# Kernel tuning notes

Hardware: AMD Instinct MI355X
Metric: run time of the kernel (lower is better)

Reference implementation:

```python
import jax, jax.numpy as jnp
import numpy as np

B, T, I = 8, 8192, 128
E, J, K = 16, 128, 1024


def setup_inputs() -> dict:
    key = jax.random.key(0)
    k1, k2, k3 = jax.random.split(key, 3)
    X = jax.random.normal(k1, (B, T, I), dtype=jnp.float32)
    ind = jax.random.randint(k2, (B, E, K), 0, T, dtype=jnp.int64)
    # matches torch.rand(E, I, J): uniform [0, 1)
    W = jax.random.uniform(k3, (E, I, J), dtype=jnp.float32)
    return {"X": X, "ind": ind, "W": W}


def reference(X, ind, W):
    # Dense per-expert matmul over ALL tokens: Y[b,e,t,j] = sum_i X[b,t,i] W[e,i,j]
    # (torch expand is a broadcast view; einsum broadcasts directly)
    Y = jnp.einsum('bti,eij->betj', X, W)  # [B, E, T, J]
    # Gather selected tokens per (batch, expert) along the token axis
    Yg = jnp.take_along_axis(Y, ind[..., None], axis=2)  # [B, E, K, J]
    return Yg
```

## Files before the change

kernel.cpp:

```cpp
#include <hip/hip_runtime.h>

#define B_ 8
#define T_ 8192
#define I_ 128
#define E_ 16
#define J_ 128
#define K_ 1024
#define ROWS 128

typedef unsigned short u16;
typedef unsigned int   u32;
typedef __attribute__((ext_vector_type(8))) short s8v;
typedef __attribute__((ext_vector_type(4))) float f4v;

__device__ __forceinline__ u16 f2bf(float f) {
    union { float f; u32 u; } v; v.f = f;
    const u32 u = v.u;
    return (u16)((u + 0x7fffu + ((u >> 16) & 1u)) >> 16);
}

__global__ __launch_bounds__(512, 4)
void gather_mfma(const float* __restrict__ X, const int* __restrict__ ind,
                 const float* __restrict__ W, float* __restrict__ Y) {
    __shared__ u16 WsT[I_ * J_];
    __shared__ u16 Xs[ROWS * I_];

    const int t    = threadIdx.x;
    const int wave = t >> 6;
    const int lane = t & 63;

    const int orig = blockIdx.x;
    const int bid  = (orig & 7) * 128 + (orig >> 3);
    const int kt = bid & 7;
    const int be = bid >> 3;
    const int e  = be & (E_ - 1);
    const int b  = be >> 4;
    const int k0 = kt * ROWS;

    const int r   = t >> 2;
    const int q   = t & 3;
    const int idx = ind[(size_t)be * K_ + k0 + r];

    {
        const float* We = W + (size_t)e * (I_ * J_);
        const int io = t & 15;
        const int j0 = (t >> 4) * 4;
        float4 w4[8];
#pragma unroll
        for (int u = 0; u < 8; ++u)
            w4[u] = *reinterpret_cast<const float4*>(We + (size_t)(io * 8 + u) * J_ + j0);
#pragma unroll
        for (int qq = 0; qq < 4; ++qq) {
            const int j = j0 + qq;
            s8v o;
#pragma unroll
            for (int u = 0; u < 8; ++u) {
                const float* wf = reinterpret_cast<const float*>(&w4[u]);
                o[u] = (short)f2bf(wf[qq]);
            }
            *reinterpret_cast<s8v*>((char*)WsT + ((j * 256 + io * 16) ^ ((j & 7) << 4))) = o;
        }
    }

    {
        const float4* Xr = reinterpret_cast<const float4*>(X + ((size_t)b * T_ + idx) * I_) + q * 8;
        const int sx = (r & 7) << 4;
        char* xrow = (char*)Xs + r * 256;
#pragma unroll
        for (int u = 0; u < 4; ++u) {
            const float4 a = Xr[2 * u], c = Xr[2 * u + 1];
            s8v o;
            o[0] = (short)f2bf(a.x); o[1] = (short)f2bf(a.y);
            o[2] = (short)f2bf(a.z); o[3] = (short)f2bf(a.w);
            o[4] = (short)f2bf(c.x); o[5] = (short)f2bf(c.y);
            o[6] = (short)f2bf(c.z); o[7] = (short)f2bf(c.w);
            *reinterpret_cast<s8v*>(xrow + ((q * 64 + u * 16) ^ sx)) = o;
        }
    }
    __syncthreads();

    const int rq  = wave >> 1;
    const int jh  = wave & 1;
    const int g   = lane >> 4;
    const int l15 = lane & 15;
    const int sx  = (lane & 7) << 4;

    const char* xb = (const char*)Xs  + (size_t)(rq * 32 + l15) * 256;
    const char* wb = (const char*)WsT + (size_t)(jh * 64 + l15) * 256;

    s8v af[2][4];
#pragma unroll
    for (int s = 0; s < 4; ++s) {
        const int off = (s * 64 + g * 16) ^ sx;
        af[0][s] = *reinterpret_cast<const s8v*>(xb + off);
        af[1][s] = *reinterpret_cast<const s8v*>(xb + 16 * 256 + off);
    }

    float* Yb = Y + ((size_t)be * K_ + k0) * J_;
#pragma unroll
    for (int n = 0; n < 4; ++n) {
        f4v acc0, acc1;
#pragma unroll
        for (int rr = 0; rr < 4; ++rr) { acc0[rr] = 0.f; acc1[rr] = 0.f; }
#pragma unroll
        for (int s = 0; s < 4; ++s) {
            const int off = (s * 64 + g * 16) ^ sx;
            const s8v bf = *reinterpret_cast<const s8v*>(wb + n * 16 * 256 + off);
            acc0 = __builtin_amdgcn_mfma_f32_16x16x32_bf16(af[0][s], bf, acc0, 0, 0, 0);
            acc1 = __builtin_amdgcn_mfma_f32_16x16x32_bf16(af[1][s], bf, acc1, 0, 0, 0);
        }
        const int col = jh * 64 + n * 16 + l15;
        const int row0 = rq * 32 + g * 4;
#pragma unroll
        for (int rr = 0; rr < 4; ++rr)
            Yb[(size_t)(row0 + rr) * J_ + col] = acc0[rr];
#pragma unroll
        for (int rr = 0; rr < 4; ++rr)
            Yb[(size_t)(row0 + 16 + rr) * J_ + col] = acc1[rr];
    }
}

extern "C" void kernel_launch(void* const* d_in, const int* in_sizes, int n_in,
                              void* d_out, int out_size, void* d_ws, size_t ws_size,
                              hipStream_t stream) {
    (void)in_sizes; (void)n_in; (void)out_size; (void)d_ws; (void)ws_size;
    const float* X   = (const float*)d_in[0];
    const int*   ind = (const int*)d_in[1];
    const float* W   = (const float*)d_in[2];
    float*       Y   = (float*)d_out;

    const int grid = B_ * E_ * (K_ / ROWS);
    hipLaunchKernelGGL(gather_mfma, dim3(grid), dim3(512), 0, stream,
                       X, ind, W, Y);
}
```

Before: 28.44 us.

## Process two row tiles per block and prefetch second X gather during compute

Each block now handles 256 token rows instead of 128, which halves the grid and amortizes the W load and bf16 transpose over twice the work. The second tile's X rows are loaded into registers before the first tile's MFMA compute and store, so the gather latency overlaps the compute. The cost is fewer blocks (512 instead of 1024), which reduces parallelism and latency hiding across CUs, plus extra registers for the prefetch buffer and two more barriers.

```diff
diff --git a/kernel.cpp b/kernel.cpp
--- a/kernel.cpp
+++ b/kernel.cpp
@@ -30,16 +30,17 @@
     const int lane = t & 63;
 
     const int orig = blockIdx.x;
-    const int bid  = (orig & 7) * 128 + (orig >> 3);
-    const int kt = bid & 7;
-    const int be = bid >> 3;
+    const int bid  = (orig & 7) * 64 + (orig >> 3);
+    const int kh = bid & 3;
+    const int be = bid >> 2;
     const int e  = be & (E_ - 1);
     const int b  = be >> 4;
-    const int k0 = kt * ROWS;
+    const int k0 = kh * (2 * ROWS);
 
     const int r   = t >> 2;
     const int q   = t & 3;
-    const int idx = ind[(size_t)be * K_ + k0 + r];
+    const int idx0 = ind[(size_t)be * K_ + k0 + r];
+    const int idx1 = ind[(size_t)be * K_ + k0 + ROWS + r];
 
     {
         const float* We = W + (size_t)e * (I_ * J_);
@@ -62,21 +63,29 @@
         }
     }
 
-    {
-        const float4* Xr = reinterpret_cast<const float4*>(X + ((size_t)b * T_ + idx) * I_) + q * 8;
-        const int sx = (r & 7) << 4;
-        char* xrow = (char*)Xs + r * 256;
+    const int sxr = (r & 7) << 4;
+    char* xrow = (char*)Xs + r * 256;
+    float4 v[8];
+    auto load_rows = [&](int idxv) {
+        const float4* Xr = reinterpret_cast<const float4*>(X + ((size_t)b * T_ + idxv) * I_) + q * 8;
+#pragma unroll
+        for (int u = 0; u < 8; ++u) v[u] = Xr[u];
+    };
+    auto pack_write = [&]() {
 #pragma unroll
         for (int u = 0; u < 4; ++u) {
-            const float4 a = Xr[2 * u], c = Xr[2 * u + 1];
+            const float4 a = v[2 * u], c = v[2 * u + 1];
             s8v o;
             o[0] = (short)f2bf(a.x); o[1] = (short)f2bf(a.y);
             o[2] = (short)f2bf(a.z); o[3] = (short)f2bf(a.w);
             o[4] = (short)f2bf(c.x); o[5] = (short)f2bf(c.y);
             o[6] = (short)f2bf(c.z); o[7] = (short)f2bf(c.w);
-            *reinterpret_cast<s8v*>(xrow + ((q * 64 + u * 16) ^ sx)) = o;
+            *reinterpret_cast<s8v*>(xrow + ((q * 64 + u * 16) ^ sxr)) = o;
         }
-    }
+    };
+
+    load_rows(idx0);
+    pack_write();
     __syncthreads();
 
     const int rq  = wave >> 1;
@@ -84,40 +93,47 @@
     const int g   = lane >> 4;
     const int l15 = lane & 15;
     const int sx  = (lane & 7) << 4;
-
     const char* xb = (const char*)Xs  + (size_t)(rq * 32 + l15) * 256;
     const char* wb = (const char*)WsT + (size_t)(jh * 64 + l15) * 256;
 
-    s8v af[2][4];
-#pragma unroll
-    for (int s = 0; s < 4; ++s) {
-        const int off = (s * 64 + g * 16) ^ sx;
-        af[0][s] = *reinterpret_cast<const s8v*>(xb + off);
-        af[1][s] = *reinterpret_cast<const s8v*>(xb + 16 * 256 + off);
-    }
-
-    float* Yb = Y + ((size_t)be * K_ + k0) * J_;
-#pragma unroll
-    for (int n = 0; n < 4; ++n) {
-        f4v acc0, acc1;
-#pragma unroll
-        for (int rr = 0; rr < 4; ++rr) { acc0[rr] = 0.f; acc1[rr] = 0.f; }
+    auto compute_store = [&](int kbase) {
+        s8v af[2][4];
 #pragma unroll
         for (int s = 0; s < 4; ++s) {
             const int off = (s * 64 + g * 16) ^ sx;
-            const s8v bf = *reinterpret_cast<const s8v*>(wb + n * 16 * 256 + off);
-            acc0 = __builtin_amdgcn_mfma_f32_16x16x32_bf16(af[0][s], bf, acc0, 0, 0, 0);
-            acc1 = __builtin_amdgcn_mfma_f32_16x16x32_bf16(af[1][s], bf, acc1, 0, 0, 0);
+            af[0][s] = *reinterpret_cast<const s8v*>(xb + off);
+            af[1][s] = *reinterpret_cast<const s8v*>(xb + 16 * 256 + off);
         }
-        const int col = jh * 64 + n * 16 + l15;
-        const int row0 = rq * 32 + g * 4;
+        float* Yb = Y + ((size_t)be * K_ + kbase) * J_;
 #pragma unroll
-        for (int rr = 0; rr < 4; ++rr)
-            Yb[(size_t)(row0 + rr) * J_ + col] = acc0[rr];
+        for (int n = 0; n < 4; ++n) {
+            f4v acc0, acc1;
 #pragma unroll
-        for (int rr = 0; rr < 4; ++rr)
-            Yb[(size_t)(row0 + 16 + rr) * J_ + col] = acc1[rr];
-    }
+            for (int rr = 0; rr < 4; ++rr) { acc0[rr] = 0.f; acc1[rr] = 0.f; }
+#pragma unroll
+            for (int s = 0; s < 4; ++s) {
+                const int off = (s * 64 + g * 16) ^ sx;
+                const s8v bf = *reinterpret_cast<const s8v*>(wb + n * 16 * 256 + off);
+                acc0 = __builtin_amdgcn_mfma_f32_16x16x32_bf16(af[0][s], bf, acc0, 0, 0, 0);
+                acc1 = __builtin_amdgcn_mfma_f32_16x16x32_bf16(af[1][s], bf, acc1, 0, 0, 0);
+            }
+            const int col = jh * 64 + n * 16 + l15;
+            const int row0 = rq * 32 + g * 4;
+#pragma unroll
+            for (int rr = 0; rr < 4; ++rr)
+                Yb[(size_t)(row0 + rr) * J_ + col] = acc0[rr];
+#pragma unroll
+            for (int rr = 0; rr < 4; ++rr)
+                Yb[(size_t)(row0 + 16 + rr) * J_ + col] = acc1[rr];
+        }
+    };
+
+    load_rows(idx1);
+    compute_store(k0);
+    __syncthreads();
+    pack_write();
+    __syncthreads();
+    compute_store(k0 + ROWS);
 }
 
 extern "C" void kernel_launch(void* const* d_in, const int* in_sizes, int n_in,
@@ -129,7 +145,7 @@
     const float* W   = (const float*)d_in[2];
     float*       Y   = (float*)d_out;
 
-    const int grid = B_ * E_ * (K_ / ROWS);
+    const int grid = B_ * E_ * (K_ / (2 * ROWS));
     hipLaunchKernelGGL(gather_mfma, dim3(grid), dim3(512), 0, stream,
                        X, ind, W, Y);
 }
```

New measurement: 28.05 us. Within noise of the previous version (-1.4%).
